# Optimization experiments

Hardware: AMD Instinct MI355X
Metric: run time of the kernel (lower is better)

The kernel has to match this reference:

```python
import jax, jax.numpy as jnp
import numpy as np


def setup_inputs() -> dict:
    key = jax.random.key(0)
    kx, kq, kk, kv = jax.random.split(key, 4)
    B, S, D = 4, 2048, 1024
    return {
        "x": jax.random.normal(kx, (B, S, D), dtype=jnp.float32),
        "Wq": jax.random.normal(kq, (D, D), dtype=jnp.float32),
        "Wk": jax.random.normal(kk, (D, D), dtype=jnp.float32),
        "Wv": jax.random.normal(kv, (D, D), dtype=jnp.float32),
    }


def reference(x, Wq, Wk, Wv):
    # x: [B, S, D]; single-head self-attention, output concat([x, attn], axis=-1)
    D = x.shape[-1]
    Q = jnp.einsum("bsd,de->bse", x, Wq)
    K = jnp.einsum("bsd,de->bse", x, Wk)
    V = jnp.einsum("bsd,de->bse", x, Wv)
    scale = 1.0 / jnp.sqrt(jnp.float32(D))
    scores = jax.nn.softmax(jnp.einsum("bqd,bkd->bqk", Q, K) * scale, axis=-1)  # [B,S,S]
    attn = jnp.einsum("bqk,bkd->bqd", scores, V)
    return jnp.concatenate([x, attn], axis=2)  # [B, S, 2D]
```

## Files before the change

kernel.cpp:

```cpp
#include <hip/hip_runtime.h>
#include <stdint.h>


typedef _Float16 h8 __attribute__((ext_vector_type(8)));
typedef _Float16 h4 __attribute__((ext_vector_type(4)));
typedef float    f4 __attribute__((ext_vector_type(4)));

__global__ __launch_bounds__(256) void prep_x_split(const float* __restrict__ x,
                                                    _Float16* __restrict__ xh,
                                                    _Float16* __restrict__ xl) {
  size_t i = (size_t)blockIdx.x * 256 + threadIdx.x;
  f4 v = ((const f4*)x)[i];
  h4 hi, lo;
#pragma unroll
  for (int j = 0; j < 4; ++j) {
    _Float16 h = (_Float16)v[j];
    hi[j] = h;
    lo[j] = (_Float16)(v[j] - (float)h);
  }
  ((h4*)xh)[i] = hi;
  ((h4*)xl)[i] = lo;
}

__global__ __launch_bounds__(256) void prep_w_split(const float* __restrict__ W,
                                                    _Float16* __restrict__ WTh,
                                                    _Float16* __restrict__ WTl) {
  int i = blockIdx.x * 256 + threadIdx.x;
  int d = i >> 10, e = i & 1023;
  float v = W[i];
  _Float16 h = (_Float16)v;
  WTh[e * 1024 + d] = h;
  if (WTl) WTl[e * 1024 + d] = (_Float16)(v - (float)h);
}

struct GemmP {
  const _Float16* Ah; const _Float16* Al;
  const _Float16* Bh; const _Float16* Bl;
  long sAz, sBz;
  int lda, ldb, K;
  float* Cf; _Float16* Ch; _Float16* Cl;
  long sCz; int ldc; float scale;
};

enum { EPI_QK = 0, EPI_VT = 1, EPI_F32 = 2 };

template <int EPI, bool SPLIT>
__global__ __launch_bounds__(256) void gemm_bt(GemmP p) {
  constexpr int BK = 64;
  constexpr int NP = SPLIT ? 4 : 2;
  __shared__ alignas(16) _Float16 sm[NP * 128 * BK];
  _Float16* sAh = sm;
  _Float16* sBh = sm + 128 * BK;

  const int t = threadIdx.x;
  const int lane = t & 63;
  const int wave = t >> 6;
  const int wm = wave >> 1, wn = wave & 1;
  const int z = blockIdx.z;

  const size_t aBase = (size_t)z * p.sAz + (size_t)blockIdx.y * 128 * p.lda;
  const size_t bBase = (size_t)z * p.sBz + (size_t)blockIdx.x * 128 * p.ldb;

  f4 acc[4][4] = {};

  const int r0 = t >> 3;
  const int s16 = t & 7;

  for (int k0 = 0; k0 < p.K; k0 += BK) {
    __syncthreads();
#pragma unroll
    for (int c = 0; c < 4; ++c) {
      int row = c * 32 + r0;
      int slot = s16 ^ (row & 7);
      int lo_ = row * BK + slot * 8;
      size_t ga = aBase + (size_t)row * p.lda + k0 + s16 * 8;
      size_t gb = bBase + (size_t)row * p.ldb + k0 + s16 * 8;
      *(h8*)&sAh[lo_] = *(const h8*)&p.Ah[ga];
      *(h8*)&sBh[lo_] = *(const h8*)&p.Bh[gb];
      if constexpr (SPLIT) {
        *(h8*)&sm[2 * 128 * BK + lo_] = *(const h8*)&p.Al[ga];
        *(h8*)&sm[3 * 128 * BK + lo_] = *(const h8*)&p.Bl[gb];
      }
    }
    __syncthreads();
#pragma unroll
    for (int ks = 0; ks < 2; ++ks) {
      h8 aH[4], bH[4], aL[4], bL[4];
#pragma unroll
      for (int m = 0; m < 4; ++m) {
        int row = wm * 64 + m * 16 + (lane & 15);
        int slot = (ks * 4 + (lane >> 4)) ^ (row & 7);
        aH[m] = *(const h8*)&sAh[row * BK + slot * 8];
        if constexpr (SPLIT) aL[m] = *(const h8*)&sm[2 * 128 * BK + row * BK + slot * 8];
      }
#pragma unroll
      for (int n = 0; n < 4; ++n) {
        int row = wn * 64 + n * 16 + (lane & 15);
        int slot = (ks * 4 + (lane >> 4)) ^ (row & 7);
        bH[n] = *(const h8*)&sBh[row * BK + slot * 8];
        if constexpr (SPLIT) bL[n] = *(const h8*)&sm[3 * 128 * BK + row * BK + slot * 8];
      }
#pragma unroll
      for (int m = 0; m < 4; ++m)
#pragma unroll
        for (int n = 0; n < 4; ++n) {
          acc[m][n] = __builtin_amdgcn_mfma_f32_16x16x32_f16(aH[m], bH[n], acc[m][n], 0, 0, 0);
          if constexpr (SPLIT) {
            acc[m][n] = __builtin_amdgcn_mfma_f32_16x16x32_f16(aH[m], bL[n], acc[m][n], 0, 0, 0);
            acc[m][n] = __builtin_amdgcn_mfma_f32_16x16x32_f16(aL[m], bH[n], acc[m][n], 0, 0, 0);
          }
        }
    }
  }

  const int gm0 = blockIdx.y * 128 + wm * 64;
  const int gn0 = blockIdx.x * 128 + wn * 64;
#pragma unroll
  for (int m = 0; m < 4; ++m) {
#pragma unroll
    for (int n = 0; n < 4; ++n) {
      int gr = gm0 + m * 16 + ((lane >> 4) << 2);
      int gc = gn0 + n * 16 + (lane & 15);
      if constexpr (EPI == EPI_QK) {
#pragma unroll
        for (int r = 0; r < 4; ++r) {
          float c = acc[m][n][r];
          _Float16 h = (_Float16)c;
          p.Ch[(size_t)(gr + r) * p.ldc + gc] = h;
          p.Cl[(size_t)(gr + r) * p.ldc + gc] = (_Float16)(c - (float)h);
        }
      } else if constexpr (EPI == EPI_VT) {
        int b = gr >> 11, s = gr & 2047;
        h4 hv;
#pragma unroll
        for (int r = 0; r < 4; ++r) hv[r] = (_Float16)acc[m][n][r];
        *(h4*)&p.Ch[(size_t)b * (1024 * 2048) + (size_t)gc * 2048 + s] = hv;
      } else {
#pragma unroll
        for (int r = 0; r < 4; ++r)
          p.Cf[(size_t)z * p.sCz + (size_t)(gr + r) * p.ldc + gc] = acc[m][n][r] * p.scale;
      }
    }
  }
}

__global__ __launch_bounds__(256) void softmax_rows(float* __restrict__ Sb) {
  const int t = threadIdx.x;
  float* row = Sb + (size_t)blockIdx.x * 2048;
  f4 v0 = ((const f4*)row)[t];
  f4 v1 = ((const f4*)row)[t + 256];
  float mx = -3.0e38f;
#pragma unroll
  for (int j = 0; j < 4; ++j) { mx = fmaxf(mx, v0[j]); mx = fmaxf(mx, v1[j]); }
#pragma unroll
  for (int o = 32; o > 0; o >>= 1) mx = fmaxf(mx, __shfl_xor(mx, o));
  __shared__ float red[4], red2[4];
  const int wave = t >> 6, lane = t & 63;
  if (lane == 0) red[wave] = mx;
  __syncthreads();
  mx = fmaxf(fmaxf(red[0], red[1]), fmaxf(red[2], red[3]));
  float pv[8];
  float sum = 0.f;
#pragma unroll
  for (int j = 0; j < 4; ++j) { pv[j] = __expf(v0[j] - mx); pv[4 + j] = __expf(v1[j] - mx); }
#pragma unroll
  for (int j = 0; j < 8; ++j) sum += pv[j];
#pragma unroll
  for (int o = 32; o > 0; o >>= 1) sum += __shfl_xor(sum, o);
  if (lane == 0) red2[wave] = sum;
  __syncthreads();
  sum = red2[0] + red2[1] + red2[2] + red2[3];
  float inv = 1.0f / sum;
  h4 o0, o1;
#pragma unroll
  for (int j = 0; j < 4; ++j) { o0[j] = (_Float16)(pv[j] * inv); o1[j] = (_Float16)(pv[4 + j] * inv); }
  _Float16* prow = (_Float16*)row;
  ((h4*)prow)[t] = o0;
  ((h4*)prow)[t + 256] = o1;
}

__global__ __launch_bounds__(256) void copy_x_half(const float* __restrict__ x,
                                                   float* __restrict__ out) {
  size_t i = (size_t)blockIdx.x * 256 + threadIdx.x;
  size_t r = i >> 8, c = i & 255;
  ((f4*)out)[r * 512 + c] = ((const f4*)x)[i];
}

__global__ void ws_sentinel(float* out, float v) { out[0] = v; }

extern "C" void kernel_launch(void* const* d_in, const int* in_sizes, int n_in,
                              void* d_out, int out_size, void* d_ws, size_t ws_size,
                              hipStream_t stream) {
  const float* x  = (const float*)d_in[0];
  const float* Wq = (const float*)d_in[1];
  const float* Wk = (const float*)d_in[2];
  const float* Wv = (const float*)d_in[3];
  float* out = (float*)d_out;

  const size_t MB = 1ull << 20;
  char* w = (char*)d_ws;
  _Float16* Qh = (_Float16*)(w + 0 * MB);
  _Float16* Ql = (_Float16*)(w + 16 * MB);
  _Float16* Kh = (_Float16*)(w + 32 * MB);
  _Float16* Kl = (_Float16*)(w + 48 * MB);
  _Float16* VT = (_Float16*)(w + 64 * MB);
  float*    S  = (float*)   (w + 80 * MB);
  _Float16* xh = (_Float16*)(w + 80 * MB);
  _Float16* xl = (_Float16*)(w + 96 * MB);
  _Float16* WqhT = (_Float16*)(w + 112 * MB);
  _Float16* WqlT = (_Float16*)(w + 114 * MB);
  _Float16* WkhT = (_Float16*)(w + 116 * MB);
  _Float16* WklT = (_Float16*)(w + 118 * MB);
  _Float16* WvhT = (_Float16*)(w + 120 * MB);

  if (ws_size < 144 * MB) {
    copy_x_half<<<8192, 256, 0, stream>>>(x, out);
    ws_sentinel<<<1, 1, 0, stream>>>(out, (float)ws_size);
    return;
  }

  prep_x_split<<<8192, 256, 0, stream>>>(x, xh, xl);
  prep_w_split<<<4096, 256, 0, stream>>>(Wq, WqhT, WqlT);
  prep_w_split<<<4096, 256, 0, stream>>>(Wk, WkhT, WklT);
  prep_w_split<<<4096, 256, 0, stream>>>(Wv, WvhT, (_Float16*)nullptr);

  GemmP pq{xh, xl, WqhT, WqlT, 0, 0, 1024, 1024, 1024,
           nullptr, Qh, Ql, 0, 1024, 1.f};
  gemm_bt<EPI_QK, true><<<dim3(8, 64, 1), 256, 0, stream>>>(pq);
  GemmP pk{xh, xl, WkhT, WklT, 0, 0, 1024, 1024, 1024,
           nullptr, Kh, Kl, 0, 1024, 1.f};
  gemm_bt<EPI_QK, true><<<dim3(8, 64, 1), 256, 0, stream>>>(pk);

  GemmP pv{xh, nullptr, WvhT, nullptr, 0, 0, 1024, 1024, 1024,
           nullptr, VT, nullptr, 0, 0, 1.f};
  gemm_bt<EPI_VT, false><<<dim3(8, 64, 1), 256, 0, stream>>>(pv);

  GemmP ps{Qh, Ql, Kh, Kl, 2048L * 1024, 2048L * 1024, 1024, 1024, 1024,
           S, nullptr, nullptr, 2048L * 2048, 2048, 0.03125f};
  gemm_bt<EPI_F32, true><<<dim3(16, 16, 4), 256, 0, stream>>>(ps);

  softmax_rows<<<8192, 256, 0, stream>>>(S);

  GemmP po{(const _Float16*)S, nullptr, VT, nullptr, 2048L * 4096, 1024L * 2048,
           4096, 2048, 2048, out + 1024, nullptr, nullptr,
           2048L * 2048, 2048, 1.f};
  gemm_bt<EPI_F32, false><<<dim3(8, 16, 4), 256, 0, stream>>>(po);

  copy_x_half<<<8192, 256, 0, stream>>>(x, out);
}
```

Measured before the change: 374.3 us.

## Replace GEMMs with pipelined 256x256 direct-to-LDS kernel and merge QKV launches

Measured after the change: 379.2 us. Within noise of the previous version (+1.3%).

```diff
diff --git a/kernel.cpp b/kernel.cpp
--- a/kernel.cpp
+++ b/kernel.cpp
@@ -6,9 +6,18 @@
 typedef _Float16 h4 __attribute__((ext_vector_type(4)));
 typedef float    f4 __attribute__((ext_vector_type(4)));
 
-__global__ __launch_bounds__(256) void prep_x_split(const float* __restrict__ x,
-                                                    _Float16* __restrict__ xh,
-                                                    _Float16* __restrict__ xl) {
+#define VMCNT(n) asm volatile("s_waitcnt vmcnt(" #n ")" ::: "memory")
+#define BAR() __builtin_amdgcn_s_barrier()
+
+__device__ __forceinline__ void gl_lds16(const _Float16* g, _Float16* l) {
+  __builtin_amdgcn_global_load_lds(
+      (const __attribute__((address_space(1))) unsigned int*)g,
+      (__attribute__((address_space(3))) unsigned int*)l, 16, 0, 0);
+}
+
+__global__ __launch_bounds__(256) void prep_x_split_copy(
+    const float* __restrict__ x, _Float16* __restrict__ xh,
+    _Float16* __restrict__ xl, float* __restrict__ out) {
   size_t i = (size_t)blockIdx.x * 256 + threadIdx.x;
   f4 v = ((const f4*)x)[i];
   h4 hi, lo;
@@ -20,6 +29,8 @@
   }
   ((h4*)xh)[i] = hi;
   ((h4*)xl)[i] = lo;
+  size_t r = i >> 8, c = i & 255;
+  ((f4*)out)[r * 512 + c] = v;
 }
 
 __global__ __launch_bounds__(256) void prep_w_split(const float* __restrict__ W,
@@ -33,114 +44,164 @@
   if (WTl) WTl[e * 1024 + d] = (_Float16)(v - (float)h);
 }
 
-struct GemmP {
-  const _Float16* Ah; const _Float16* Al;
-  const _Float16* Bh; const _Float16* Bl;
-  long sAz, sBz;
-  int lda, ldb, K;
-  float* Cf; _Float16* Ch; _Float16* Cl;
-  long sCz; int ldc; float scale;
+enum { EM_F32 = 0, EM_QK = 1, EM_VT = 2 };
+
+struct G8 {
+  const _Float16* Areg[3]; long zA; int lda;
+  const _Float16* Breg[4][3]; long zB; int ldb;
+  int NT[4];
+  int emode[4];
+  float* Cf; long zC; int ldc; float scale;
+  _Float16* Ch[4]; _Float16* Cl[4];
+  _Float16* Vt;
 };
 
-enum { EPI_QK = 0, EPI_VT = 1, EPI_F32 = 2 };
-
-template <int EPI, bool SPLIT>
-__global__ __launch_bounds__(256) void gemm_bt(GemmP p) {
-  constexpr int BK = 64;
-  constexpr int NP = SPLIT ? 4 : 2;
-  __shared__ alignas(16) _Float16 sm[NP * 128 * BK];
-  _Float16* sAh = sm;
-  _Float16* sBh = sm + 128 * BK;
-
+__global__ __launch_bounds__(512) void gemm8p(G8 p) {
+  __shared__ alignas(16) _Float16 lds[2][2][256][64];
   const int t = threadIdx.x;
   const int lane = t & 63;
-  const int wave = t >> 6;
-  const int wm = wave >> 1, wn = wave & 1;
+  const int w = t >> 6;
+  const int wm = w >> 2, wn = w & 3;
+  const int l15 = lane & 15, l4 = lane >> 4;
   const int z = blockIdx.z;
-
-  const size_t aBase = (size_t)z * p.sAz + (size_t)blockIdx.y * 128 * p.lda;
-  const size_t bBase = (size_t)z * p.sBz + (size_t)blockIdx.x * 128 * p.ldb;
-
-  f4 acc[4][4] = {};
-
-  const int r0 = t >> 3;
-  const int s16 = t & 7;
-
-  for (int k0 = 0; k0 < p.K; k0 += BK) {
-    __syncthreads();
-#pragma unroll
-    for (int c = 0; c < 4; ++c) {
-      int row = c * 32 + r0;
-      int slot = s16 ^ (row & 7);
-      int lo_ = row * BK + slot * 8;
-      size_t ga = aBase + (size_t)row * p.lda + k0 + s16 * 8;
-      size_t gb = bBase + (size_t)row * p.ldb + k0 + s16 * 8;
-      *(h8*)&sAh[lo_] = *(const h8*)&p.Ah[ga];
-      *(h8*)&sBh[lo_] = *(const h8*)&p.Bh[gb];
-      if constexpr (SPLIT) {
-        *(h8*)&sm[2 * 128 * BK + lo_] = *(const h8*)&p.Al[ga];
-        *(h8*)&sm[3 * 128 * BK + lo_] = *(const h8*)&p.Bl[gb];
+  const long Mb = (long)blockIdx.y * 256;
+  const long Nb = (long)blockIdx.x * 256;
+  const int nt = p.NT[z];
+  const long zAo = p.zA * z;
+  const long zBo = p.zB * z;
+  const int lda = p.lda, ldb = p.ldb;
+
+  const int rr_lo = t >> 3;
+  const int slot = t & 7;
+  const int rr0_lo = (t & ~63) >> 3;
+
+  f4 acc[8][4] = {};
+
+  auto stage = [&](int u, int sb, int kt) {
+    const int k0 = kt << 6;
+    const int r = k0 >> 10;
+    const int cn = k0 & 1023;
+    const _Float16* Ab = p.Areg[r] + zAo + cn;
+    const _Float16* Bb = p.Breg[z][r] + zBo + cn;
+#pragma unroll
+    for (int i = 0; i < 2; ++i) {
+      int rr = i * 64 + rr_lo;
+      int rr0 = i * 64 + rr0_lo;
+      if (u == 0 || u == 3) {
+        int qm = (u == 3);
+        int row  = ((rr  >> 6) << 7) | (qm << 6) | (rr  & 63);
+        int row0 = ((rr0 >> 6) << 7) | (qm << 6) | (rr0 & 63);
+        int scol = (slot ^ (row & 7)) << 3;
+        gl_lds16(Ab + (Mb + row) * (long)lda + scol, &lds[sb][0][row0][0]);
+      } else {
+        int qn = (u == 2);
+        int row  = ((rr  >> 5) << 6) | (qn << 5) | (rr  & 31);
+        int row0 = ((rr0 >> 5) << 6) | (qn << 5) | (rr0 & 31);
+        int scol = (slot ^ (row & 7)) << 3;
+        gl_lds16(Bb + (Nb + row) * (long)ldb + scol, &lds[sb][1][row0][0]);
       }
     }
-    __syncthreads();
-#pragma unroll
-    for (int ks = 0; ks < 2; ++ks) {
-      h8 aH[4], bH[4], aL[4], bL[4];
-#pragma unroll
-      for (int m = 0; m < 4; ++m) {
-        int row = wm * 64 + m * 16 + (lane & 15);
-        int slot = (ks * 4 + (lane >> 4)) ^ (row & 7);
-        aH[m] = *(const h8*)&sAh[row * BK + slot * 8];
-        if constexpr (SPLIT) aL[m] = *(const h8*)&sm[2 * 128 * BK + row * BK + slot * 8];
+  };
+
+  auto phase = [&](int q, int kt, bool dostage) {
+    const int buf = kt & 1;
+    const int qm = q >> 1, qn = q & 1;
+    h8 af[4][2];
+    h8 bf[2][2];
+#pragma unroll
+    for (int m = 0; m < 4; ++m) {
+      int row = wm * 128 + (qm * 4 + m) * 16 + l15;
+#pragma unroll
+      for (int ks = 0; ks < 2; ++ks)
+        af[m][ks] = *(const h8*)&lds[buf][0][row][(((ks * 4 + l4) ^ (row & 7)) << 3)];
+    }
+#pragma unroll
+    for (int n = 0; n < 2; ++n) {
+      int row = wn * 64 + (qn * 2 + n) * 16 + l15;
+#pragma unroll
+      for (int ks = 0; ks < 2; ++ks)
+        bf[n][ks] = *(const h8*)&lds[buf][1][row][(((ks * 4 + l4) ^ (row & 7)) << 3)];
+    }
+    if (dostage) stage(q, buf ^ 1, kt + 1);
+    __builtin_amdgcn_s_barrier();
+    asm volatile("s_waitcnt lgkmcnt(0)" ::: "memory");
+    __builtin_amdgcn_sched_barrier(0);
+    __builtin_amdgcn_s_setprio(1);
+#pragma unroll
+    for (int ks = 0; ks < 2; ++ks)
+#pragma unroll
+      for (int m = 0; m < 4; ++m)
+#pragma unroll
+        for (int n = 0; n < 2; ++n)
+          acc[qm * 4 + m][qn * 2 + n] = __builtin_amdgcn_mfma_f32_16x16x32_f16(
+              af[m][ks], bf[n][ks], acc[qm * 4 + m][qn * 2 + n], 0, 0, 0);
+    __builtin_amdgcn_s_setprio(0);
+  };
+
+  stage(0, 0, 0); stage(1, 0, 0); stage(2, 0, 0); stage(3, 0, 0);
+  VMCNT(4);
+  BAR();
+
+  for (int kt = 0; kt < nt - 1; ++kt) {
+    phase(0, kt, true);  VMCNT(4); BAR();
+    phase(1, kt, true);  VMCNT(4); BAR();
+    phase(2, kt, true);            BAR();
+    phase(3, kt, true);  VMCNT(4); BAR();
+  }
+  {
+    int kt = nt - 1;
+    phase(0, kt, false); VMCNT(2); BAR();
+    phase(1, kt, false); VMCNT(0); BAR();
+    phase(2, kt, false);           BAR();
+    phase(3, kt, false);
+  }
+
+  const int em = p.emode[z];
+  const long gr0 = wm * 128 + l4 * 4;
+  const long gc0 = wn * 64 + l15;
+  if (em == EM_F32) {
+    float* C = p.Cf + p.zC * z;
+#pragma unroll
+    for (int i = 0; i < 8; ++i)
+#pragma unroll
+      for (int j = 0; j < 4; ++j) {
+        long gr = Mb + gr0 + i * 16;
+        long gc = Nb + gc0 + j * 16;
+#pragma unroll
+        for (int r = 0; r < 4; ++r)
+          C[(gr + r) * (long)p.ldc + gc] = acc[i][j][r] * p.scale;
       }
-#pragma unroll
-      for (int n = 0; n < 4; ++n) {
-        int row = wn * 64 + n * 16 + (lane & 15);
-        int slot = (ks * 4 + (lane >> 4)) ^ (row & 7);
-        bH[n] = *(const h8*)&sBh[row * BK + slot * 8];
-        if constexpr (SPLIT) bL[n] = *(const h8*)&sm[3 * 128 * BK + row * BK + slot * 8];
+  } else if (em == EM_QK) {
+    _Float16* Ch = p.Ch[z];
+    _Float16* Cl = p.Cl[z];
+#pragma unroll
+    for (int i = 0; i < 8; ++i)
+#pragma unroll
+      for (int j = 0; j < 4; ++j) {
+        long gr = Mb + gr0 + i * 16;
+        long gc = Nb + gc0 + j * 16;
+#pragma unroll
+        for (int r = 0; r < 4; ++r) {
+          float c = acc[i][j][r];
+          _Float16 h = (_Float16)c;
+          Ch[(gr + r) * 1024 + gc] = h;
+          Cl[(gr + r) * 1024 + gc] = (_Float16)(c - (float)h);
+        }
       }
-#pragma unroll
-      for (int m = 0; m < 4; ++m)
-#pragma unroll
-        for (int n = 0; n < 4; ++n) {
-          acc[m][n] = __builtin_amdgcn_mfma_f32_16x16x32_f16(aH[m], bH[n], acc[m][n], 0, 0, 0);
-          if constexpr (SPLIT) {
-            acc[m][n] = __builtin_amdgcn_mfma_f32_16x16x32_f16(aH[m], bL[n], acc[m][n], 0, 0, 0);
-            acc[m][n] = __builtin_amdgcn_mfma_f32_16x16x32_f16(aL[m], bH[n], acc[m][n], 0, 0, 0);
-          }
-        }
-    }
-  }
-
-  const int gm0 = blockIdx.y * 128 + wm * 64;
-  const int gn0 = blockIdx.x * 128 + wn * 64;
-#pragma unroll
-  for (int m = 0; m < 4; ++m) {
-#pragma unroll
-    for (int n = 0; n < 4; ++n) {
-      int gr = gm0 + m * 16 + ((lane >> 4) << 2);
-      int gc = gn0 + n * 16 + (lane & 15);
-      if constexpr (EPI == EPI_QK) {
-#pragma unroll
-        for (int r = 0; r < 4; ++r) {
-          float c = acc[m][n][r];
-          _Float16 h = (_Float16)c;
-          p.Ch[(size_t)(gr + r) * p.ldc + gc] = h;
-          p.Cl[(size_t)(gr + r) * p.ldc + gc] = (_Float16)(c - (float)h);
-        }
-      } else if constexpr (EPI == EPI_VT) {
-        int b = gr >> 11, s = gr & 2047;
+  } else {
+    _Float16* Vt = p.Vt;
+#pragma unroll
+    for (int i = 0; i < 8; ++i)
+#pragma unroll
+      for (int j = 0; j < 4; ++j) {
+        long gr = Mb + gr0 + i * 16;
+        long gc = Nb + gc0 + j * 16;
+        long b = gr >> 11, s = gr & 2047;
         h4 hv;
 #pragma unroll
-        for (int r = 0; r < 4; ++r) hv[r] = (_Float16)acc[m][n][r];
-        *(h4*)&p.Ch[(size_t)b * (1024 * 2048) + (size_t)gc * 2048 + s] = hv;
-      } else {
-#pragma unroll
-        for (int r = 0; r < 4; ++r)
-          p.Cf[(size_t)z * p.sCz + (size_t)(gr + r) * p.ldc + gc] = acc[m][n][r] * p.scale;
+        for (int r = 0; r < 4; ++r) hv[r] = (_Float16)acc[i][j][r];
+        *(h4*)&Vt[b * (long)(1024 * 2048) + gc * 2048 + s] = hv;
       }
-    }
   }
 }
 
@@ -219,32 +280,45 @@
     return;
   }
 
-  prep_x_split<<<8192, 256, 0, stream>>>(x, xh, xl);
+  prep_x_split_copy<<<8192, 256, 0, stream>>>(x, xh, xl, out);
   prep_w_split<<<4096, 256, 0, stream>>>(Wq, WqhT, WqlT);
   prep_w_split<<<4096, 256, 0, stream>>>(Wk, WkhT, WklT);
   prep_w_split<<<4096, 256, 0, stream>>>(Wv, WvhT, (_Float16*)nullptr);
 
-  GemmP pq{xh, xl, WqhT, WqlT, 0, 0, 1024, 1024, 1024,
-           nullptr, Qh, Ql, 0, 1024, 1.f};
-  gemm_bt<EPI_QK, true><<<dim3(8, 64, 1), 256, 0, stream>>>(pq);
-  GemmP pk{xh, xl, WkhT, WklT, 0, 0, 1024, 1024, 1024,
-           nullptr, Kh, Kl, 0, 1024, 1.f};
-  gemm_bt<EPI_QK, true><<<dim3(8, 64, 1), 256, 0, stream>>>(pk);
-
-  GemmP pv{xh, nullptr, WvhT, nullptr, 0, 0, 1024, 1024, 1024,
-           nullptr, VT, nullptr, 0, 0, 1.f};
-  gemm_bt<EPI_VT, false><<<dim3(8, 64, 1), 256, 0, stream>>>(pv);
-
-  GemmP ps{Qh, Ql, Kh, Kl, 2048L * 1024, 2048L * 1024, 1024, 1024, 1024,
-           S, nullptr, nullptr, 2048L * 2048, 2048, 0.03125f};
-  gemm_bt<EPI_F32, true><<<dim3(16, 16, 4), 256, 0, stream>>>(ps);
+  G8 pp = {};
+  pp.Areg[0] = xh; pp.Areg[1] = xl; pp.Areg[2] = xh; pp.zA = 0; pp.lda = 1024;
+  pp.Breg[0][0] = WqhT; pp.Breg[0][1] = WqhT; pp.Breg[0][2] = WqlT;
+  pp.Breg[1][0] = WkhT; pp.Breg[1][1] = WkhT; pp.Breg[1][2] = WklT;
+  pp.Breg[2][0] = WvhT; pp.Breg[2][1] = WvhT; pp.Breg[2][2] = WvhT;
+  pp.zB = 0; pp.ldb = 1024;
+  pp.NT[0] = 48; pp.NT[1] = 48; pp.NT[2] = 16;
+  pp.emode[0] = EM_QK; pp.emode[1] = EM_QK; pp.emode[2] = EM_VT;
+  pp.Ch[0] = Qh; pp.Cl[0] = Ql; pp.Ch[1] = Kh; pp.Cl[1] = Kl;
+  pp.Vt = VT;
+  gemm8p<<<dim3(4, 32, 3), 512, 0, stream>>>(pp);
+
+  G8 ps = {};
+  ps.Areg[0] = Qh; ps.Areg[1] = Ql; ps.Areg[2] = Qh;
+  ps.zA = 2048L * 1024; ps.lda = 1024;
+  for (int zz = 0; zz < 4; ++zz) {
+    ps.Breg[zz][0] = Kh; ps.Breg[zz][1] = Kh; ps.Breg[zz][2] = Kl;
+    ps.NT[zz] = 48; ps.emode[zz] = EM_F32;
+  }
+  ps.zB = 2048L * 1024; ps.ldb = 1024;
+  ps.Cf = S; ps.zC = 2048L * 2048; ps.ldc = 2048; ps.scale = 0.03125f;
+  gemm8p<<<dim3(8, 8, 4), 512, 0, stream>>>(ps);
 
   softmax_rows<<<8192, 256, 0, stream>>>(S);
 
-  GemmP po{(const _Float16*)S, nullptr, VT, nullptr, 2048L * 4096, 1024L * 2048,
-           4096, 2048, 2048, out + 1024, nullptr, nullptr,
-           2048L * 2048, 2048, 1.f};
-  gemm_bt<EPI_F32, false><<<dim3(8, 16, 4), 256, 0, stream>>>(po);
-
-  copy_x_half<<<8192, 256, 0, stream>>>(x, out);
-}
+  G8 po = {};
+  const _Float16* P = (const _Float16*)S;
+  po.Areg[0] = P; po.Areg[1] = P + 1024; po.Areg[2] = P;
+  po.zA = 2048L * 4096; po.lda = 4096;
+  for (int zz = 0; zz < 4; ++zz) {
+    po.Breg[zz][0] = VT; po.Breg[zz][1] = VT + 1024; po.Breg[zz][2] = VT;
+    po.NT[zz] = 32; po.emode[zz] = EM_F32;
+  }
+  po.zB = 1024L * 2048; po.ldb = 2048;
+  po.Cf = out + 1024; po.zC = 2048L * 2048; po.ldc = 2048; po.scale = 1.f;
+  gemm8p<<<dim3(4, 8, 4), 512, 0, stream>>>(po);
+}
```
